# Performance work log

Measured on AMD Instinct MI355X. Metric: run time of the kernel, lower is better.

Reference implementation:

```python
import jax, jax.numpy as jnp
import numpy as np


def _normalized_adj(A):
    # get_a: d = 0.5*I, a = off-diagonal ones + A, a2 = d @ a @ d
    off = jnp.array([[0., 1., 1.], [1., 0., 1.], [1., 1., 0.]], dtype=A.dtype)
    a = off + A
    d = 0.5 * jnp.eye(3, dtype=A.dtype)
    return d @ a @ d  # [3,3]


def setup_inputs() -> dict:
    key = jax.random.key(0)
    k1, k2 = jax.random.split(key)
    B = 8192
    x = jax.random.normal(k1, (B, 3, 10), dtype=jnp.float32)
    A = jnp.eye(3, dtype=jnp.float32)  # get_A() returns identity; Parameter init
    stdv = 1.0 / np.sqrt(10.0)
    W = jax.random.uniform(k2, (10, 10), dtype=jnp.float32, minval=-stdv, maxval=stdv)
    return {"x": x, "A": A, "W": W}


def reference(x, A, W):
    # adjacency is detached in the torch forward
    adj = jax.lax.stop_gradient(_normalized_adj(A))  # [3,3], shared across batch
    # GraphConvolution: adj @ (x @ W)
    support = jnp.einsum('bnf,fo->bno', x, W)          # [B,3,10]
    h = jnp.einsum('nm,bmo->bno', adj, support)        # [B,3,10]
    # permute -> [B,10,3]; AvgPool1d(2) on length 3 -> length 1: mean of nodes 0,1
    pooled = 0.5 * (h[:, 0, :] + h[:, 1, :])           # [B,10]
    # ScaleDotProductAttention over the batch axis
    score = jax.nn.softmax(pooled @ pooled.T, axis=-1)  # [B,B]
    v = score @ pooled                                  # [B,10]
    return v
```

## Files before the change

kernel.cpp:

```cpp
#include <hip/hip_runtime.h>
#include <math.h>

#define BROWS 8192
#define F 10
#define NT 16
#define NW 16
#define IB 16
#define SQRT_LOG2E 1.2011224087864498f

#if __has_builtin(__builtin_amdgcn_exp2f)
#define EXP2F(x) __builtin_amdgcn_exp2f(x)
#else
#define EXP2F(x) exp2f(x)
#endif

typedef _Float16 half4 __attribute__((ext_vector_type(4)));
typedef __fp16 fp16x2 __attribute__((ext_vector_type(2)));
typedef float floatx4 __attribute__((ext_vector_type(4)));

__device__ __forceinline__ half4 exp4_to_h4(float a, float b, float c, float d) {
#if __has_builtin(__builtin_amdgcn_cvt_pkrtz)
    union { fp16x2 h2[2]; half4 h4; } u;
    u.h2[0] = __builtin_amdgcn_cvt_pkrtz(EXP2F(a), EXP2F(b));
    u.h2[1] = __builtin_amdgcn_cvt_pkrtz(EXP2F(c), EXP2F(d));
    return u.h4;
#else
    half4 r;
    r[0] = (_Float16)EXP2F(a); r[1] = (_Float16)EXP2F(b);
    r[2] = (_Float16)EXP2F(c); r[3] = (_Float16)EXP2F(d);
    return r;
#endif
}

__device__ __forceinline__ uint32_t pack2(_Float16 a, _Float16 b) {
    union { _Float16 h[2]; uint32_t u; } x;
    x.h[0] = a; x.h[1] = b;
    return x.u;
}

__device__ __forceinline__ void gload_lds16(const void* g, void* l) {
#if __has_builtin(__builtin_amdgcn_global_load_lds)
    __builtin_amdgcn_global_load_lds(
        (const __attribute__((address_space(1))) void*)g,
        (__attribute__((address_space(3))) void*)l, 16, 0, 0);
#else
    *(float4*)l = *(const float4*)g;
#endif
}

__device__ __forceinline__ void wait_vm0() {
#if __has_builtin(__builtin_amdgcn_s_waitcnt)
    __builtin_amdgcn_s_waitcnt(0x0F70);
#endif
}

__device__ __forceinline__ void sched_fence() {
#if __has_builtin(__builtin_amdgcn_sched_barrier)
    __builtin_amdgcn_sched_barrier(0);
#endif
}

__global__ void pooled_kernel(const float* __restrict__ x,
                              const float* __restrict__ A,
                              const float* __restrict__ W,
                              _Float16* __restrict__ q_tiled,
                              _Float16* __restrict__ a_tiled) {
    int b = blockIdx.x * blockDim.x + threadIdx.x;
    if (b >= BROWS) return;

    float c0 = 0.125f * (1.0f + A[0] + A[3]);
    float c1 = 0.125f * (1.0f + A[1] + A[4]);
    float c2 = 0.125f * (2.0f + A[2] + A[5]);

    const float2* xb = (const float2*)(x + (size_t)b * 3 * F);
    float xv[3 * F];
#pragma unroll
    for (int k = 0; k < 15; ++k) {
        float2 t = xb[k];
        xv[2 * k] = t.x; xv[2 * k + 1] = t.y;
    }

    float y[F];
#pragma unroll
    for (int f = 0; f < F; ++f)
        y[f] = c0 * xv[f] + c1 * xv[F + f] + c2 * xv[2 * F + f];

    float po[F];
#pragma unroll
    for (int o = 0; o < F; ++o) {
        float acc = 0.0f;
#pragma unroll
        for (int f = 0; f < F; ++f)
            acc = fmaf(y[f], W[f * F + o], acc);
        po[o] = acc;
    }

    float s = SQRT_LOG2E;
    uint2* qd = (uint2*)(q_tiled + (size_t)b * 16);
    qd[0] = make_uint2(pack2((_Float16)(s*po[0]), (_Float16)(s*po[1])),
                       pack2((_Float16)(s*po[2]), (_Float16)(s*po[3])));
    qd[1] = make_uint2(pack2((_Float16)(s*po[4]), (_Float16)(s*po[5])),
                       pack2((_Float16)(s*po[6]), (_Float16)(s*po[7])));
    qd[2] = make_uint2(pack2((_Float16)(s*po[8]), (_Float16)(s*po[9])), 0u);
    qd[3] = make_uint2(0u, 0u);

    _Float16* at = a_tiled + (size_t)(b >> 5) * 512 + (b & 31);
#pragma unroll
    for (int o = 0; o < F; ++o)
        at[o * 32] = (_Float16)po[o];
    at[10 * 32] = (_Float16)1.0f;
#pragma unroll
    for (int o = 11; o < 16; ++o)
        at[o * 32] = (_Float16)0.0f;
}

__global__ void attn_kernel(const _Float16* __restrict__ q_tiled,
                            const _Float16* __restrict__ a_tiled,
                            float* __restrict__ out) {
    __shared__ __align__(16) _Float16 ring[2][NW][1024];
    float* red = (float*)&ring[0][0][0];

    const int tid  = threadIdx.x;
    const int wave = tid >> 6;
    const int lane = tid & 63;
    const int m    = lane & 15;
    const int quad = lane >> 4;
    const int i0   = blockIdx.x * IB;

    half4 b1 = *(const half4*)(q_tiled + (size_t)(i0 + m) * 16 + quad * 4);

    const char* qsrc = (const char*)q_tiled + (size_t)wave * 1024 + lane * 16;
    const char* asrc = (const char*)a_tiled + (size_t)wave * 1024 + lane * 16;

    char* slot[2] = { (char*)&ring[0][wave][0] + lane * 16,
                      (char*)&ring[1][wave][0] + lane * 16 };

    floatx4 acc0 = {0.f,0.f,0.f,0.f}, acc1 = {0.f,0.f,0.f,0.f};

    gload_lds16(qsrc, slot[0]);
    gload_lds16(asrc + 0x40000  - 0x40000, slot[0] + 1024);
    qsrc += 16 * 1024; asrc += 16 * 1024;

    for (int t = 0; t < NT; ++t) {
        const int buf = t & 1;
        const _Float16* qs = &ring[buf][wave][0];
        const _Float16* as_ = qs + 512;

        wait_vm0();
        half4 a1_0 = *(const half4*)&qs[(0 * 16 + m) * 16 + quad * 4];
        half4 ag_0 = *(const half4*)&as_[m * 32 + 0 * 16 + quad * 4];
        half4 a1_1 = *(const half4*)&qs[(1 * 16 + m) * 16 + quad * 4];
        half4 ag_1 = *(const half4*)&as_[m * 32 + 1 * 16 + quad * 4];
        sched_fence();

        if (t + 1 < NT) {
            gload_lds16(qsrc, slot[buf ^ 1]);
            gload_lds16(asrc, slot[buf ^ 1] + 1024);
            qsrc += 16 * 1024; asrc += 16 * 1024;
        }

        floatx4 d1a = __builtin_amdgcn_mfma_f32_16x16x16f16(
            a1_0, b1, (floatx4){0.f,0.f,0.f,0.f}, 0, 0, 0);
        floatx4 d1b = __builtin_amdgcn_mfma_f32_16x16x16f16(
            a1_1, b1, (floatx4){0.f,0.f,0.f,0.f}, 0, 0, 0);
        half4 a2a = exp4_to_h4(d1a[0], d1a[1], d1a[2], d1a[3]);
        half4 a2b = exp4_to_h4(d1b[0], d1b[1], d1b[2], d1b[3]);
        acc0 = __builtin_amdgcn_mfma_f32_16x16x16f16(ag_0, a2a, acc0, 0, 0, 0);
        acc1 = __builtin_amdgcn_mfma_f32_16x16x16f16(ag_1, a2b, acc1, 0, 0, 0);
    }

    floatx4 acc = acc0 + acc1;

    __syncthreads();
    if (quad < 3)
        *(floatx4*)&red[((size_t)wave * IB + m) * 12 + quad * 4] = acc;
    __syncthreads();

    if (tid < IB * F) {
        const int i = tid / F;
        const int f = tid % F;
        float sum = 0.0f, l = 0.0f;
#pragma unroll
        for (int w = 0; w < NW; ++w) {
            sum += red[((size_t)w * IB + i) * 12 + f];
            l   += red[((size_t)w * IB + i) * 12 + 10];
        }
        out[(size_t)(i0 + i) * F + f] = sum / l;
    }
}

extern "C" void kernel_launch(void* const* d_in, const int* in_sizes, int n_in,
                              void* d_out, int out_size, void* d_ws, size_t ws_size,
                              hipStream_t stream) {
    const float* x = (const float*)d_in[0];
    const float* A = (const float*)d_in[1];
    const float* W = (const float*)d_in[2];
    float* out = (float*)d_out;

    _Float16* q_tiled = (_Float16*)d_ws;
    _Float16* a_tiled = (_Float16*)((char*)d_ws + 262144);

    pooled_kernel<<<BROWS / 64, 64, 0, stream>>>(x, A, W, q_tiled, a_tiled);
    attn_kernel<<<BROWS / IB, NW * 64, 0, stream>>>(q_tiled, a_tiled, out);
}
```

Before: 82.26 us.

## Process 32 query rows per block and deepen LDS prefetch ring to four stages

Each block now handles two 16-row query tiles, so every key/value tile staged in LDS is reused for twice as many MFMA and exp operations, and half as many blocks are launched. The double-buffered global-to-LDS ring becomes a four-slot ring with three tiles in flight, using partial vmcnt waits instead of a full drain each iteration. The explicit scheduling barrier is removed. This adds register pressure and LDS (128KB ring) and leaves fewer blocks (256) to spread across CUs.

Measured after the change: 69.13 us. 1.19x faster.

```diff
diff --git a/kernel.cpp b/kernel.cpp
--- a/kernel.cpp
+++ b/kernel.cpp
@@ -5,7 +5,7 @@
 #define F 10
 #define NT 16
 #define NW 16
-#define IB 16
+#define IB 32
 #define SQRT_LOG2E 1.2011224087864498f
 
 #if __has_builtin(__builtin_amdgcn_exp2f)
@@ -13,6 +13,8 @@
 #else
 #define EXP2F(x) exp2f(x)
 #endif
+
+#define WAITVM(n) __builtin_amdgcn_s_waitcnt(0xF00 | 0x70 | (n))
 
 typedef _Float16 half4 __attribute__((ext_vector_type(4)));
 typedef __fp16 fp16x2 __attribute__((ext_vector_type(2)));
@@ -48,18 +50,6 @@
 #endif
 }
 
-__device__ __forceinline__ void wait_vm0() {
-#if __has_builtin(__builtin_amdgcn_s_waitcnt)
-    __builtin_amdgcn_s_waitcnt(0x0F70);
-#endif
-}
-
-__device__ __forceinline__ void sched_fence() {
-#if __has_builtin(__builtin_amdgcn_sched_barrier)
-    __builtin_amdgcn_sched_barrier(0);
-#endif
-}
-
 __global__ void pooled_kernel(const float* __restrict__ x,
                               const float* __restrict__ A,
                               const float* __restrict__ W,
@@ -117,7 +107,7 @@
 __global__ void attn_kernel(const _Float16* __restrict__ q_tiled,
                             const _Float16* __restrict__ a_tiled,
                             float* __restrict__ out) {
-    __shared__ __align__(16) _Float16 ring[2][NW][1024];
+    __shared__ __align__(16) _Float16 ring[4][NW][1024];
     float* red = (float*)&ring[0][0][0];
 
     const int tid  = threadIdx.x;
@@ -127,53 +117,68 @@
     const int quad = lane >> 4;
     const int i0   = blockIdx.x * IB;
 
-    half4 b1 = *(const half4*)(q_tiled + (size_t)(i0 + m) * 16 + quad * 4);
+    half4 b1a = *(const half4*)(q_tiled + (size_t)(i0 + m) * 16 + quad * 4);
+    half4 b1b = *(const half4*)(q_tiled + (size_t)(i0 + 16 + m) * 16 + quad * 4);
 
     const char* qsrc = (const char*)q_tiled + (size_t)wave * 1024 + lane * 16;
     const char* asrc = (const char*)a_tiled + (size_t)wave * 1024 + lane * 16;
 
-    char* slot[2] = { (char*)&ring[0][wave][0] + lane * 16,
-                      (char*)&ring[1][wave][0] + lane * 16 };
-
-    floatx4 acc0 = {0.f,0.f,0.f,0.f}, acc1 = {0.f,0.f,0.f,0.f};
-
-    gload_lds16(qsrc, slot[0]);
-    gload_lds16(asrc + 0x40000  - 0x40000, slot[0] + 1024);
-    qsrc += 16 * 1024; asrc += 16 * 1024;
+    char* slotp[4];
+#pragma unroll
+    for (int s = 0; s < 4; ++s)
+        slotp[s] = (char*)&ring[s][wave][0] + lane * 16;
+
+#pragma unroll
+    for (int s = 0; s < 3; ++s) {
+        gload_lds16(qsrc, slotp[s]);
+        gload_lds16(asrc, slotp[s] + 1024);
+        qsrc += 16 * 1024; asrc += 16 * 1024;
+    }
+
+    floatx4 accA0 = {0.f,0.f,0.f,0.f}, accA1 = {0.f,0.f,0.f,0.f};
+    floatx4 accB0 = {0.f,0.f,0.f,0.f}, accB1 = {0.f,0.f,0.f,0.f};
 
     for (int t = 0; t < NT; ++t) {
-        const int buf = t & 1;
-        const _Float16* qs = &ring[buf][wave][0];
+        if (t < NT - 2)      WAITVM(4);
+        else if (t == NT-2)  WAITVM(2);
+        else                 WAITVM(0);
+
+        const _Float16* qs  = &ring[t & 3][wave][0];
         const _Float16* as_ = qs + 512;
-
-        wait_vm0();
         half4 a1_0 = *(const half4*)&qs[(0 * 16 + m) * 16 + quad * 4];
+        half4 a1_1 = *(const half4*)&qs[(1 * 16 + m) * 16 + quad * 4];
         half4 ag_0 = *(const half4*)&as_[m * 32 + 0 * 16 + quad * 4];
-        half4 a1_1 = *(const half4*)&qs[(1 * 16 + m) * 16 + quad * 4];
         half4 ag_1 = *(const half4*)&as_[m * 32 + 1 * 16 + quad * 4];
-        sched_fence();
-
-        if (t + 1 < NT) {
-            gload_lds16(qsrc, slot[buf ^ 1]);
-            gload_lds16(asrc, slot[buf ^ 1] + 1024);
+
+        if (t + 3 < NT) {
+            gload_lds16(qsrc, slotp[(t + 3) & 3]);
+            gload_lds16(asrc, slotp[(t + 3) & 3] + 1024);
             qsrc += 16 * 1024; asrc += 16 * 1024;
         }
 
-        floatx4 d1a = __builtin_amdgcn_mfma_f32_16x16x16f16(
-            a1_0, b1, (floatx4){0.f,0.f,0.f,0.f}, 0, 0, 0);
-        floatx4 d1b = __builtin_amdgcn_mfma_f32_16x16x16f16(
-            a1_1, b1, (floatx4){0.f,0.f,0.f,0.f}, 0, 0, 0);
-        half4 a2a = exp4_to_h4(d1a[0], d1a[1], d1a[2], d1a[3]);
-        half4 a2b = exp4_to_h4(d1b[0], d1b[1], d1b[2], d1b[3]);
-        acc0 = __builtin_amdgcn_mfma_f32_16x16x16f16(ag_0, a2a, acc0, 0, 0, 0);
-        acc1 = __builtin_amdgcn_mfma_f32_16x16x16f16(ag_1, a2b, acc1, 0, 0, 0);
-    }
-
-    floatx4 acc = acc0 + acc1;
+        floatx4 z = {0.f,0.f,0.f,0.f};
+        floatx4 d1a0 = __builtin_amdgcn_mfma_f32_16x16x16f16(a1_0, b1a, z, 0, 0, 0);
+        floatx4 d1b0 = __builtin_amdgcn_mfma_f32_16x16x16f16(a1_0, b1b, z, 0, 0, 0);
+        floatx4 d1a1 = __builtin_amdgcn_mfma_f32_16x16x16f16(a1_1, b1a, z, 0, 0, 0);
+        floatx4 d1b1 = __builtin_amdgcn_mfma_f32_16x16x16f16(a1_1, b1b, z, 0, 0, 0);
+        half4 a2a0 = exp4_to_h4(d1a0[0], d1a0[1], d1a0[2], d1a0[3]);
+        half4 a2b0 = exp4_to_h4(d1b0[0], d1b0[1], d1b0[2], d1b0[3]);
+        half4 a2a1 = exp4_to_h4(d1a1[0], d1a1[1], d1a1[2], d1a1[3]);
+        half4 a2b1 = exp4_to_h4(d1b1[0], d1b1[1], d1b1[2], d1b1[3]);
+        accA0 = __builtin_amdgcn_mfma_f32_16x16x16f16(ag_0, a2a0, accA0, 0, 0, 0);
+        accB0 = __builtin_amdgcn_mfma_f32_16x16x16f16(ag_0, a2b0, accB0, 0, 0, 0);
+        accA1 = __builtin_amdgcn_mfma_f32_16x16x16f16(ag_1, a2a1, accA1, 0, 0, 0);
+        accB1 = __builtin_amdgcn_mfma_f32_16x16x16f16(ag_1, a2b1, accB1, 0, 0, 0);
+    }
+
+    floatx4 accA = accA0 + accA1;
+    floatx4 accB = accB0 + accB1;
 
     __syncthreads();
-    if (quad < 3)
-        *(floatx4*)&red[((size_t)wave * IB + m) * 12 + quad * 4] = acc;
+    if (quad < 3) {
+        *(floatx4*)&red[((size_t)wave * IB + m) * 12 + quad * 4] = accA;
+        *(floatx4*)&red[((size_t)wave * IB + 16 + m) * 12 + quad * 4] = accB;
+    }
     __syncthreads();
 
     if (tid < IB * F) {
```
